# Optimization experiments

Measured on AMD Instinct MI355X. Metric: run time of the kernel, lower is better.

## Reference

```python
import jax, jax.numpy as jnp
import numpy as np

LOCAL = (1, 2, 2, 2)
NUM_HEADS = 8


def conv4d(x, w, b):
    # x: (B, L, C, D, H, W); w: (Cout, Cin, 3) temporal conv, 'same' padding on L.
    L = x.shape[1]
    xp = jnp.pad(x, ((0, 0), (1, 1), (0, 0), (0, 0), (0, 0), (0, 0)))
    y = (jnp.einsum('blcdhw,oc->blodhw', xp[:, 0:L], w[:, :, 0])
         + jnp.einsum('blcdhw,oc->blodhw', xp[:, 1:L + 1], w[:, :, 1])
         + jnp.einsum('blcdhw,oc->blodhw', xp[:, 2:L + 2], w[:, :, 2]))
    return y + b[None, None, :, None, None, None]


def to_windows(x):
    # (B, L, C, D, H, W) -> (B, nlw, heads, ws, hd)
    B, L, C, D, H, W = x.shape
    l0, l1, l2, l3 = LOCAL
    nl, nd, nh, nw = L // l0, D // l1, H // l2, W // l3
    x = jnp.transpose(x, (0, 2, 1, 3, 4, 5))  # B C L D H W
    x = x.reshape(B, C, nl, l0, nd, l1, nh, l2, nw, l3)
    x = jnp.transpose(x, (0, 2, 4, 6, 8, 3, 5, 7, 9, 1))  # B nl nd nh nw l0 l1 l2 l3 C
    nlw, ws = nl * nd * nh * nw, l0 * l1 * l2 * l3
    x = x.reshape(B, nlw, ws, NUM_HEADS, C // NUM_HEADS)
    return jnp.transpose(x, (0, 1, 3, 2, 4))


def from_windows(y, shape):
    # (B, nlw, heads, ws, hd) -> (B, L, C, D, H, W)
    B, L, C, D, H, W = shape
    l0, l1, l2, l3 = LOCAL
    nl, nd, nh, nw = L // l0, D // l1, H // l2, W // l3
    y = jnp.transpose(y, (0, 1, 3, 2, 4)).reshape(B, nl, nd, nh, nw, l0, l1, l2, l3, C)
    y = jnp.transpose(y, (0, 9, 1, 5, 2, 6, 3, 7, 4, 8)).reshape(B, C, L, D, H, W)
    return jnp.transpose(y, (0, 2, 1, 3, 4, 5))


def window_attn(q, k, v, scale):
    attn = jax.nn.softmax(jnp.einsum('bnhqd,bnhkd->bnhqk', q, k) * scale, axis=-1)
    return jnp.einsum('bnhqk,bnhkd->bnhqd', attn, v)


def tlg_forward(x, wq, bq, wk, bk, wv, bv, wp, bp):
    B, L, C, D, H, W = x.shape
    scale = (C // NUM_HEADS) ** (-0.5)
    half_shape = (B, L // 2, C, D, H, W)
    xs, xe = x[:, :L // 2], x[:, L // 2:]
    # start-queries attend to end keys/values
    qs = to_windows(conv4d(xs, wq, bq))
    ke = to_windows(conv4d(xe, wk, bk))
    ve = to_windows(conv4d(xe, wv, bv))
    yse = from_windows(window_attn(qs, ke, ve, scale), half_shape)
    yse = conv4d(yse, wp, bp)
    # end-queries attend to start keys/values
    qe = to_windows(conv4d(xe, wq, bq))
    ks = to_windows(conv4d(xs, wk, bk))
    vs = to_windows(conv4d(xs, wv, bv))
    yes = from_windows(window_attn(qe, ks, vs, scale), half_shape)
    yes = conv4d(yes, wp, bp)
    return jnp.concatenate([yse, yes], axis=1)


def setup_inputs() -> dict:
    key = jax.random.key(0)
    ks = jax.random.split(key, 10)
    C = 128
    wscale = 1.0 / np.sqrt(C * 3)
    x = jax.random.normal(ks[0], (2, 8, C, 16, 32, 32), dtype=jnp.float32)
    def w(k):
        return jax.random.normal(k, (C, C, 3), dtype=jnp.float32) * wscale
    def b(k):
        return jax.random.normal(k, (C,), dtype=jnp.float32) * 0.01
    return {
        'x': x,
        'wq': w(ks[1]), 'bq': b(ks[2]),
        'wk': w(ks[3]), 'bk': b(ks[4]),
        'wv': w(ks[5]), 'bv': b(ks[6]),
        'wp': w(ks[7]), 'bp': b(ks[8]),
    }


def reference(x, wq, bq, wk, bk, wv, bv, wp, bp):
    return tlg_forward(x, wq, bq, wk, bk, wv, bv, wp, bp)
```

## Files before the change

### kernel.cpp

```cpp
#include <hip/hip_runtime.h>

typedef __attribute__((ext_vector_type(8))) short short8;
typedef __attribute__((ext_vector_type(4))) float v4f;

#define C_CH 128
#define S_SP 16384
#define NSLICE 16
#define KTOT 384

__device__ inline float bf2f(unsigned short u) {
  union { unsigned int i; float f; } v; v.i = ((unsigned int)u) << 16; return v.f;
}
__device__ inline unsigned short f2bf(float f) {
  union { float f; unsigned int i; } v; v.f = f;
  unsigned int u = v.i;
  return (unsigned short)((u + 0x7FFFu + ((u >> 16) & 1u)) >> 16);
}

__device__ inline void gload_lds16(const unsigned short* g, unsigned short* l) {
  __builtin_amdgcn_global_load_lds(
      (const __attribute__((address_space(1))) void*)g,
      (__attribute__((address_space(3))) void*)l, 16, 0, 0);
}

__global__ __launch_bounds__(256) void repack_kernel(
    const float* __restrict__ wq, const float* __restrict__ wk,
    const float* __restrict__ wv, const float* __restrict__ wp,
    const float* __restrict__ bq, const float* __restrict__ bk,
    const float* __restrict__ bv, const float* __restrict__ bp,
    unsigned short* __restrict__ Wr, float* __restrict__ biasf)
{
  int i = blockIdx.x * 256 + threadIdx.x;
  const int WN = 4 * 49152;
  if (i < WN) {
    int m = i / 49152;
    int r = i % 49152;
    int o = r / 384, k = r % 384;
    int t = k >> 7, c = k & 127;
    const float* w = (m == 0) ? wq : (m == 1) ? wk : (m == 2) ? wv : wp;
    Wr[i] = f2bf(w[o * 384 + c * 3 + t]);
  } else if (i < WN + 512) {
    int j = i - WN;
    int m = j >> 7, o = j & 127;
    const float* bb = (m == 0) ? bq : (m == 1) ? bk : (m == 2) ? bv : bp;
    biasf[j] = bb[o];
  }
}

__global__ __launch_bounds__(256) void transpose_f2b_kernel(
    const float* __restrict__ in, unsigned short* __restrict__ out,
    int R, int C)
{
  __shared__ unsigned short t[64][72];
  int tid = threadIdx.x;
  size_t slice = blockIdx.z;
  const float* ip = in + slice * (size_t)R * C;
  unsigned short* op = out + slice * (size_t)R * C;
  int c0 = blockIdx.x * 64, r0 = blockIdx.y * 64;
#pragma unroll
  for (int p = 0; p < 4; ++p) {
    int id = tid + p * 256;
    int row = id >> 4, col = (id & 15) * 4;
    float4 v = *(const float4*)(ip + (size_t)(r0 + row) * C + c0 + col);
    t[row][col + 0] = f2bf(v.x);
    t[row][col + 1] = f2bf(v.y);
    t[row][col + 2] = f2bf(v.z);
    t[row][col + 3] = f2bf(v.w);
  }
  __syncthreads();
#pragma unroll
  for (int p = 0; p < 2; ++p) {
    int id = tid + p * 256;
    int crow = id >> 3, rcol = (id & 7) * 8;
    uint4 v;
    v.x = (unsigned)t[rcol + 0][crow] | ((unsigned)t[rcol + 1][crow] << 16);
    v.y = (unsigned)t[rcol + 2][crow] | ((unsigned)t[rcol + 3][crow] << 16);
    v.z = (unsigned)t[rcol + 4][crow] | ((unsigned)t[rcol + 5][crow] << 16);
    v.w = (unsigned)t[rcol + 6][crow] | ((unsigned)t[rcol + 7][crow] << 16);
    *(uint4*)(op + (size_t)(c0 + crow) * R + r0 + rcol) = v;
  }
}

__global__ __launch_bounds__(256) void transpose_b2f_kernel(
    const unsigned short* __restrict__ in, float* __restrict__ out,
    int R, int C)
{
  __shared__ unsigned short t[64][72];
  int tid = threadIdx.x;
  size_t slice = blockIdx.z;
  const unsigned short* ip = in + slice * (size_t)R * C;
  float* op = out + slice * (size_t)R * C;
  int c0 = blockIdx.x * 64, r0 = blockIdx.y * 64;
#pragma unroll
  for (int p = 0; p < 2; ++p) {
    int id = tid + p * 256;
    int row = id >> 3, col = (id & 7) * 8;
    uint4 v = *(const uint4*)(ip + (size_t)(r0 + row) * C + c0 + col);
    *(uint4*)(&t[row][col]) = v;
  }
  __syncthreads();
#pragma unroll
  for (int p = 0; p < 4; ++p) {
    int id = tid + p * 256;
    int crow = id >> 4, rcol = (id & 15) * 4;
    float4 v;
    v.x = bf2f(t[rcol + 0][crow]);
    v.y = bf2f(t[rcol + 1][crow]);
    v.z = bf2f(t[rcol + 2][crow]);
    v.w = bf2f(t[rcol + 3][crow]);
    *(float4*)(op + (size_t)(c0 + crow) * R + r0 + rcol) = v;
  }
}

__global__ __launch_bounds__(256) void conv_mfma_kernel(
    const unsigned short* __restrict__ inT,
    const unsigned short* __restrict__ Wr_all,
    const float* __restrict__ bias_all,
    unsigned short* __restrict__ outT_all)
{
  __shared__ unsigned short Blds[2][128 * 64];

  int z = blockIdx.z;
  const unsigned short* Wr = Wr_all + (size_t)z * 49152;
  const float* bias = bias_all + z * 128;
  unsigned short* outT = outT_all + (size_t)z * NSLICE * S_SP * C_CH;

  int tid = threadIdx.x;
  int s0 = blockIdx.x * 128;
  int slice = blockIdx.y;
  int b = slice >> 3, l = slice & 7;
  int lh = l & 3;
  int t_lo = (lh == 0) ? 1 : 0;
  int t_hi = (lh == 3) ? 1 : 2;
  int ap_hi = t_hi * 2 + 1;

  int w = tid >> 6, lane = tid & 63;
  int quad = lane >> 4, l15 = lane & 15;

  short8 af[2][12];
#pragma unroll
  for (int i = 0; i < 2; ++i)
#pragma unroll
    for (int k = 0; k < 12; ++k)
      af[i][k] = *(const short8*)(Wr + (w * 32 + i * 16 + l15) * KTOT + k * 32 + quad * 8);

  v4f acc[2][8];
#pragma unroll
  for (int i = 0; i < 2; ++i)
#pragma unroll
    for (int j = 0; j < 8; ++j)
      acc[i][j] = (v4f){0.f, 0.f, 0.f, 0.f};

  int srow_i = lane >> 3;
  int scs = (lane & 7) ^ srow_i;

  auto STAGE = [&](int t, int sub, int bsel) {
    int lp = l - 1 + t;
    const unsigned short* gb =
        inT + ((size_t)(b * 8 + lp) * S_SP + s0) * C_CH + sub * 64;
#pragma unroll
    for (int q = 0; q < 4; ++q) {
      int row = (w * 4 + q) * 8 + srow_i;
      gload_lds16(gb + (size_t)row * C_CH + scs * 8,
                  &Blds[bsel][(w * 4 + q) * 512]);
    }
  };

  STAGE(t_lo, 0, 0);
  asm volatile("s_waitcnt vmcnt(0)" ::: "memory");
  __builtin_amdgcn_s_barrier();

#pragma unroll
  for (int ap = 0; ap < 6; ++ap) {
    int t = ap >> 1, sub = ap & 1;
    if (t < t_lo || t > t_hi) continue;

    if (ap + 1 <= ap_hi)
      STAGE((ap + 1) >> 1, (ap + 1) & 1, (ap + 1) & 1);

    const unsigned short* Bp = &Blds[ap & 1][0];
#pragma unroll
    for (int ks = 0; ks < 2; ++ks) {
      short8 bfr[8];
#pragma unroll
      for (int j = 0; j < 8; ++j) {
        int srow = j * 16 + l15;
        int cs = (ks * 4 + quad) ^ (l15 & 7);
        bfr[j] = *(const short8*)(Bp + srow * 64 + cs * 8);
      }
#pragma unroll
      for (int i = 0; i < 2; ++i)
#pragma unroll
        for (int j = 0; j < 8; ++j)
          acc[i][j] = __builtin_amdgcn_mfma_f32_16x16x32_bf16(
              af[i][t * 4 + sub * 2 + ks], bfr[j], acc[i][j], 0, 0, 0);
    }
    asm volatile("s_waitcnt vmcnt(0)" ::: "memory");
    __builtin_amdgcn_s_barrier();
  }

#pragma unroll
  for (int i = 0; i < 2; ++i) {
    int obase = w * 32 + i * 16 + quad * 4;
    float4 bb = *(const float4*)(bias + obase);
#pragma unroll
    for (int j = 0; j < 8; ++j) {
      int s = s0 + j * 16 + l15;
      float f0 = acc[i][j].x + bb.x;
      float f1 = acc[i][j].y + bb.y;
      float f2 = acc[i][j].z + bb.z;
      float f3 = acc[i][j].w + bb.w;
      uint2 st;
      st.x = (unsigned)f2bf(f0) | ((unsigned)f2bf(f1) << 16);
      st.y = (unsigned)f2bf(f2) | ((unsigned)f2bf(f3) << 16);
      *(uint2*)(outT + ((size_t)slice * S_SP + s) * C_CH + obase) = st;
    }
  }
}

__device__ inline void load16(const unsigned short* p, float* f) {
  uint4 a = *(const uint4*)p;
  uint4 c = *(const uint4*)(p + 8);
  unsigned v[8] = {a.x, a.y, a.z, a.w, c.x, c.y, c.z, c.w};
#pragma unroll
  for (int i = 0; i < 8; ++i) {
    f[2 * i] = bf2f((unsigned short)(v[i] & 0xffffu));
    f[2 * i + 1] = bf2f((unsigned short)(v[i] >> 16));
  }
}

__global__ __launch_bounds__(256) void attn_kernel(
    const unsigned short* __restrict__ QT,
    const unsigned short* __restrict__ KT,
    const unsigned short* __restrict__ VT,
    unsigned short* __restrict__ YT)
{
  int tid = threadIdx.x;
  int wave = tid >> 6, lane = tid & 63;
  int dir = wave & 1;
  int win = blockIdx.x * 2 + (wave >> 1);
  int by = blockIdx.y;
  int b = by >> 2, l0 = by & 3;
  int head = lane >> 3, qi = lane & 7;
  int d0 = win >> 8, h0 = (win >> 4) & 15, w0 = win & 15;
  int lq = l0 + dir * 4;
  int lk = l0 + 4 - dir * 4;
  int sE[8];
#pragma unroll
  for (int e = 0; e < 8; ++e)
    sE[e] = (2 * d0 + (e >> 2)) * 1024 + (2 * h0 + ((e >> 1) & 1)) * 32 + (2 * w0 + (e & 1));

  size_t qbase = ((size_t)(b * 8 + lq) * S_SP + sE[qi]) * C_CH + head * 16;
  size_t kslice = (size_t)(b * 8 + lk) * S_SP;
  float q[16];
  load16(QT + qbase, q);

  float lg[8];
#pragma unroll
  for (int j = 0; j < 8; ++j) {
    float kk[16];
    load16(KT + (kslice + sE[j]) * C_CH + head * 16, kk);
    float d = 0.f;
#pragma unroll
    for (int x = 0; x < 16; ++x) d += q[x] * kk[x];
    lg[j] = d * 0.25f;
  }
  float m = lg[0];
#pragma unroll
  for (int j = 1; j < 8; ++j) m = fmaxf(m, lg[j]);
  float p[8], sum = 0.f;
#pragma unroll
  for (int j = 0; j < 8; ++j) { p[j] = __expf(lg[j] - m); sum += p[j]; }
  float inv = 1.0f / sum;

  float y[16];
#pragma unroll
  for (int x = 0; x < 16; ++x) y[x] = 0.f;
#pragma unroll
  for (int j = 0; j < 8; ++j) {
    float vv[16];
    load16(VT + (kslice + sE[j]) * C_CH + head * 16, vv);
    float pj = p[j] * inv;
#pragma unroll
    for (int x = 0; x < 16; ++x) y[x] += pj * vv[x];
  }
  uint4 o0, o1;
  o0.x = (unsigned)f2bf(y[0]) | ((unsigned)f2bf(y[1]) << 16);
  o0.y = (unsigned)f2bf(y[2]) | ((unsigned)f2bf(y[3]) << 16);
  o0.z = (unsigned)f2bf(y[4]) | ((unsigned)f2bf(y[5]) << 16);
  o0.w = (unsigned)f2bf(y[6]) | ((unsigned)f2bf(y[7]) << 16);
  o1.x = (unsigned)f2bf(y[8]) | ((unsigned)f2bf(y[9]) << 16);
  o1.y = (unsigned)f2bf(y[10]) | ((unsigned)f2bf(y[11]) << 16);
  o1.z = (unsigned)f2bf(y[12]) | ((unsigned)f2bf(y[13]) << 16);
  o1.w = (unsigned)f2bf(y[14]) | ((unsigned)f2bf(y[15]) << 16);
  *(uint4*)(YT + qbase) = o0;
  *(uint4*)(YT + qbase + 8) = o1;
}

extern "C" void kernel_launch(void* const* d_in, const int* in_sizes, int n_in,
                              void* d_out, int out_size, void* d_ws, size_t ws_size,
                              hipStream_t stream) {
  const float* x  = (const float*)d_in[0];
  const float* wq = (const float*)d_in[1];
  const float* bq = (const float*)d_in[2];
  const float* wk = (const float*)d_in[3];
  const float* bk = (const float*)d_in[4];
  const float* wv = (const float*)d_in[5];
  const float* bv = (const float*)d_in[6];
  const float* wp = (const float*)d_in[7];
  const float* bp = (const float*)d_in[8];

  char* ws = (char*)d_ws;
  unsigned short* Wr = (unsigned short*)ws;
  float* biasf = (float*)(ws + 393216);
  size_t off = 395264;
  const size_t TENB = (size_t)NSLICE * S_SP * C_CH * 2;
  unsigned short* xT = (unsigned short*)(ws + off); off += TENB;
  unsigned short* QT = (unsigned short*)(ws + off); off += TENB;
  unsigned short* KT = (unsigned short*)(ws + off); off += TENB;
  unsigned short* VT = (unsigned short*)(ws + off); off += TENB;
  unsigned short* YT = xT;
  unsigned short* OT = QT;

  hipLaunchKernelGGL(repack_kernel, dim3(770), dim3(256), 0, stream,
                     wq, wk, wv, wp, bq, bk, bv, bp, Wr, biasf);
  hipLaunchKernelGGL(transpose_f2b_kernel, dim3(256, 2, 16), dim3(256), 0, stream,
                     x, xT, 128, 16384);
  hipLaunchKernelGGL(conv_mfma_kernel, dim3(128, 16, 3), dim3(256), 0, stream,
                     xT, Wr, biasf, QT);
  hipLaunchKernelGGL(attn_kernel, dim3(1024, 8), dim3(256), 0, stream,
                     QT, KT, VT, YT);
  hipLaunchKernelGGL(conv_mfma_kernel, dim3(128, 16, 1), dim3(256), 0, stream,
                     YT, Wr + 3 * 49152, biasf + 384, OT);
  hipLaunchKernelGGL(transpose_b2f_kernel, dim3(2, 256, 16), dim3(256), 0, stream,
                     OT, (float*)d_out, 16384, 128);
}
```

Measured before the change: 534.8 us.

## Triple-buffer conv LDS staging and stream weight fragments per phase

The temporal-conv MFMA kernel moves from double to triple LDS buffering, prefetching two phases ahead and using partial vmcnt waits instead of a full drain each step. Weight fragments are no longer all loaded into 48 registers upfront; each phase's 4 fragments are loaded just before use, rotating through three register sets. This lowers register pressure (launch bounds now request 3 blocks per SM) and overlaps global loads with MFMA work. In exchange the kernel uses more LDS per block and has more complex wait counting.

```diff
diff --git a/kernel.cpp b/kernel.cpp
--- a/kernel.cpp
+++ b/kernel.cpp
@@ -112,13 +112,13 @@
   }
 }
 
-__global__ __launch_bounds__(256) void conv_mfma_kernel(
+__global__ __launch_bounds__(256, 3) void conv_mfma_kernel(
     const unsigned short* __restrict__ inT,
     const unsigned short* __restrict__ Wr_all,
     const float* __restrict__ bias_all,
     unsigned short* __restrict__ outT_all)
 {
-  __shared__ unsigned short Blds[2][128 * 64];
+  __shared__ unsigned short Blds[3][128 * 64];
 
   int z = blockIdx.z;
   const unsigned short* Wr = Wr_all + (size_t)z * 49152;
@@ -132,17 +132,12 @@
   int lh = l & 3;
   int t_lo = (lh == 0) ? 1 : 0;
   int t_hi = (lh == 3) ? 1 : 2;
-  int ap_hi = t_hi * 2 + 1;
+  int lo = t_lo * 2, hi = t_hi * 2 + 1;
 
   int w = tid >> 6, lane = tid & 63;
   int quad = lane >> 4, l15 = lane & 15;
-
-  short8 af[2][12];
-#pragma unroll
-  for (int i = 0; i < 2; ++i)
-#pragma unroll
-    for (int k = 0; k < 12; ++k)
-      af[i][k] = *(const short8*)(Wr + (w * 32 + i * 16 + l15) * KTOT + k * 32 + quad * 8);
+  int srow_i = lane >> 3;
+  int scs = (lane & 7) ^ srow_i;
 
   v4f acc[2][8];
 #pragma unroll
@@ -151,53 +146,77 @@
     for (int j = 0; j < 8; ++j)
       acc[i][j] = (v4f){0.f, 0.f, 0.f, 0.f};
 
-  int srow_i = lane >> 3;
-  int scs = (lane & 7) ^ srow_i;
-
-  auto STAGE = [&](int t, int sub, int bsel) {
-    int lp = l - 1 + t;
-    const unsigned short* gb =
-        inT + ((size_t)(b * 8 + lp) * S_SP + s0) * C_CH + sub * 64;
-#pragma unroll
-    for (int q = 0; q < 4; ++q) {
-      int row = (w * 4 + q) * 8 + srow_i;
-      gload_lds16(gb + (size_t)row * C_CH + scs * 8,
-                  &Blds[bsel][(w * 4 + q) * 512]);
-    }
-  };
-
-  STAGE(t_lo, 0, 0);
-  asm volatile("s_waitcnt vmcnt(0)" ::: "memory");
-  __builtin_amdgcn_s_barrier();
-
-#pragma unroll
-  for (int ap = 0; ap < 6; ++ap) {
-    int t = ap >> 1, sub = ap & 1;
-    if (t < t_lo || t > t_hi) continue;
-
-    if (ap + 1 <= ap_hi)
-      STAGE((ap + 1) >> 1, (ap + 1) & 1, (ap + 1) & 1);
-
-    const unsigned short* Bp = &Blds[ap & 1][0];
-#pragma unroll
-    for (int ks = 0; ks < 2; ++ks) {
-      short8 bfr[8];
-#pragma unroll
-      for (int j = 0; j < 8; ++j) {
-        int srow = j * 16 + l15;
-        int cs = (ks * 4 + quad) ^ (l15 & 7);
-        bfr[j] = *(const short8*)(Bp + srow * 64 + cs * 8);
-      }
-#pragma unroll
-      for (int i = 0; i < 2; ++i)
-#pragma unroll
-        for (int j = 0; j < 8; ++j)
-          acc[i][j] = __builtin_amdgcn_mfma_f32_16x16x32_bf16(
-              af[i][t * 4 + sub * 2 + ks], bfr[j], acc[i][j], 0, 0, 0);
-    }
-    asm volatile("s_waitcnt vmcnt(0)" ::: "memory");
-    __builtin_amdgcn_s_barrier();
-  }
+  short8 af0[4], af1[4], af2[4];
+
+#define STAGE(ap, bsel) do {                                                   \
+    int t_ = (ap) >> 1;                                                        \
+    const unsigned short* gb_ =                                                \
+        inT + ((size_t)(b * 8 + l - 1 + t_) * S_SP + s0) * C_CH +              \
+        ((ap) & 1) * 64;                                                       \
+    _Pragma("unroll")                                                          \
+    for (int q_ = 0; q_ < 4; ++q_)                                             \
+      gload_lds16(gb_ + (size_t)((w * 4 + q_) * 8 + srow_i) * C_CH + scs * 8,  \
+                  &Blds[bsel][(w * 4 + q_) * 512]);                            \
+  } while (0)
+
+#define AFLOAD(ap, set) do {                                                   \
+    _Pragma("unroll")                                                          \
+    for (int i_ = 0; i_ < 2; ++i_)                                             \
+      _Pragma("unroll")                                                        \
+      for (int ks_ = 0; ks_ < 2; ++ks_)                                        \
+        set[i_ * 2 + ks_] = *(const short8*)(                                  \
+            Wr + (size_t)(w * 32 + i_ * 16 + l15) * KTOT +                     \
+            (ap) * 64 + ks_ * 32 + quad * 8);                                  \
+  } while (0)
+
+  if (lo == 0) {
+    STAGE(0, 0); AFLOAD(0, af0);
+    __builtin_amdgcn_sched_barrier(0);
+    STAGE(1, 1); AFLOAD(1, af1);
+  } else {
+    STAGE(2, 2); AFLOAD(2, af2);
+    __builtin_amdgcn_sched_barrier(0);
+    STAGE(3, 0); AFLOAD(3, af0);
+  }
+
+#define PHASE(ap, CURSET, NXTSET)                                              \
+  if ((ap) >= lo && (ap) <= hi) {                                              \
+    if ((ap) == hi) { asm volatile("s_waitcnt vmcnt(0)" ::: "memory"); }       \
+    else            { asm volatile("s_waitcnt vmcnt(8)" ::: "memory"); }       \
+    __builtin_amdgcn_s_barrier();                                              \
+    if ((ap) + 2 <= hi) { STAGE((ap) + 2, ((ap) + 2) % 3);                     \
+                          AFLOAD((ap) + 2, NXTSET); }                          \
+    const unsigned short* Bp_ = &Blds[(ap) % 3][0];                            \
+    _Pragma("unroll")                                                          \
+    for (int ks = 0; ks < 2; ++ks) {                                           \
+      _Pragma("unroll")                                                        \
+      for (int jg = 0; jg < 2; ++jg) {                                         \
+        short8 bfr[4];                                                         \
+        _Pragma("unroll")                                                      \
+        for (int j4 = 0; j4 < 4; ++j4)                                         \
+          bfr[j4] = *(const short8*)(                                          \
+              Bp_ + ((jg * 4 + j4) * 16 + l15) * 64 +                          \
+              (((ks * 4 + quad) ^ (l15 & 7)) * 8));                            \
+        _Pragma("unroll")                                                      \
+        for (int i = 0; i < 2; ++i)                                            \
+          _Pragma("unroll")                                                    \
+          for (int j4 = 0; j4 < 4; ++j4)                                       \
+            acc[i][jg * 4 + j4] = __builtin_amdgcn_mfma_f32_16x16x32_bf16(     \
+                CURSET[i * 2 + ks], bfr[j4], acc[i][jg * 4 + j4], 0, 0, 0);    \
+      }                                                                        \
+    }                                                                          \
+  }
+
+  PHASE(0, af0, af2)
+  PHASE(1, af1, af0)
+  PHASE(2, af2, af1)
+  PHASE(3, af0, af2)
+  PHASE(4, af1, af0)
+  PHASE(5, af2, af0)
+
+#undef PHASE
+#undef AFLOAD
+#undef STAGE
 
 #pragma unroll
   for (int i = 0; i < 2; ++i) {
```

After: 490.6 us. 1.09x faster.
